# Kernel optimization log

Hardware: AMD Instinct MI355X
Metric: run time of the kernel (lower is better)

The kernel has to match this reference:

```python
import jax, jax.numpy as jnp
import numpy as np

# irreps layout: list of (multiplicity, l); same for input and output (square Linear)
IRREPS = [(256, 0), (128, 1), (64, 2)]  # dims: 256 + 384 + 320 = 960
N_NODES = 100000
N_TRIVIAL = 256  # dim of leading 0e block in irreps_out


def setup_inputs() -> dict:
    key = jax.random.key(0)
    ks = jax.random.split(key, 5)
    data_in = jax.random.normal(ks[0], (N_NODES, sum(m * (2 * l + 1) for m, l in IRREPS)), dtype=jnp.float32)
    # weight init matching linear_layer_init: uniform(-a, a), a = sqrt(6/(mul1*mul2 + mul_out)),
    # here mul1 = mul_out = mul, mul2 = 1 -> a = sqrt(6 / (2*mul)) = sqrt(3/mul)
    Ws = {}
    for i, (mul, l) in enumerate(IRREPS):
        a = float(np.sqrt(3.0 / mul))
        Ws[f"W{i}"] = jax.random.uniform(ks[i + 1], (mul, mul), minval=-a, maxval=a, dtype=jnp.float32)
    b = jnp.zeros((N_TRIVIAL,), dtype=jnp.float32)
    return {"data_in": data_in, "W0": Ws["W0"], "W1": Ws["W1"], "W2": Ws["W2"], "b": b}


def reference(data_in, W0, W1, W2, b):
    # FullyConnectedTensorProduct(irreps_in, '1x0e', irreps_out) with x2 = ones reduces to
    # per-irrep block matmul: out_block = (x_block @ W) / sqrt(mul_in)
    # (w3j(l,0,l) = I/sqrt(2l+1) cancels with component-norm sqrt((2l+1)/mul_in)).
    Ws = [W0, W1, W2]
    outs = []
    off = 0
    for (mul, l), W in zip(IRREPS, Ws):
        d = 2 * l + 1
        x = data_in[:, off : off + mul * d].reshape(-1, mul, d)  # [N, mul, 2l+1]
        y = jnp.einsum("bud,uw->bwd", x, W) * (1.0 / np.sqrt(mul))
        outs.append(y.reshape(-1, mul * d))
        off += mul * d
    out = jnp.concatenate(outs, axis=1)
    # bias added only to the leading trivial (0e) block
    out = out.at[:, :N_TRIVIAL].add(b)
    return out
```

## Files before the change

kernel.cpp:

```cpp
#include <hip/hip_runtime.h>

typedef __attribute__((ext_vector_type(8))) short short8;
typedef __attribute__((ext_vector_type(4))) float f32x4;

__device__ __forceinline__ unsigned pack2bf(float x0, float x1) {
    unsigned u0 = __float_as_uint(x0) + 0x8000u;
    unsigned u1 = __float_as_uint(x1) + 0x8000u;
    return __builtin_amdgcn_perm(u1, u0, 0x07060302u);
}

__global__ __launch_bounds__(256) void prep_w(const float* __restrict__ W,
                                              unsigned short* __restrict__ dst,
                                              int mul, float scale) {
    int idx = blockIdx.x * 256 + threadIdx.x;
    if (idx >= mul * mul) return;
    int u = idx >> (mul == 256 ? 8 : (mul == 128 ? 7 : 6));
    int w = idx - u * mul;
    int nkb = mul >> 5;
    int cb = w >> 4, kb = u >> 5;
    int lane = ((u >> 3) & 3) * 16 + (w & 15);
    int j = u & 7;
    unsigned uv = __float_as_uint(W[idx] * scale) + 0x8000u;
    dst[(((cb * nkb + kb) * 64 + lane) << 3) + j] = (unsigned short)(uv >> 16);
}

template <int MUL, int D, int OFF, bool BIAS>
__device__ __forceinline__ void do_block(const float* __restrict__ inA0,
                                         float* __restrict__ outb,
                                         const unsigned short* __restrict__ wf,
                                         int lm, int lg, int lane,
                                         const float* __restrict__ bias) {
    constexpr int NKB = MUL / 32;
    constexpr int NCB = MUL / 16;
    short8 a[D][NKB];
    const float* rowp = inA0 + OFF;
#pragma unroll
    for (int kb = 0; kb < NKB; ++kb) {
        float buf[8 * D];
        const float* p = rowp + (kb * 32 + lg * 8) * D;
#pragma unroll
        for (int v = 0; v < 2 * D; ++v) {
            f32x4 t = *reinterpret_cast<const f32x4*>(p + v * 4);
            buf[v * 4 + 0] = t[0]; buf[v * 4 + 1] = t[1];
            buf[v * 4 + 2] = t[2]; buf[v * 4 + 3] = t[3];
        }
#pragma unroll
        for (int d = 0; d < D; ++d) {
            union { short8 s8; unsigned u32[4]; } fr;
#pragma unroll
            for (int jj = 0; jj < 4; ++jj)
                fr.u32[jj] = pack2bf(buf[(2 * jj) * D + d], buf[(2 * jj + 1) * D + d]);
            a[d][kb] = fr.s8;
        }
    }
#pragma unroll 2
    for (int cb = 0; cb < NCB; ++cb) {
        short8 bfr[NKB];
#pragma unroll
        for (int kb = 0; kb < NKB; ++kb)
            bfr[kb] = *reinterpret_cast<const short8*>(wf + (((cb * NKB + kb) * 64 + lane) << 3));
        float bv = BIAS ? bias[cb * 16 + lm] : 0.0f;
        f32x4 acc[D];
#pragma unroll
        for (int d = 0; d < D; ++d) {
            f32x4 z = {0.0f, 0.0f, 0.0f, 0.0f};
#pragma unroll
            for (int kb = 0; kb < NKB; ++kb)
                z = __builtin_amdgcn_mfma_f32_16x16x32_bf16(a[d][kb], bfr[kb], z, 0, 0, 0);
            acc[d] = z;
        }
#pragma unroll
        for (int jj = 0; jj < 4; ++jj) {
            float* op = outb + (lg * 4 + jj) * 960 + OFF + (cb * 16 + lm) * D;
#pragma unroll
            for (int d = 0; d < D; ++d)
                op[d] = BIAS ? (acc[d][jj] + bv) : acc[d][jj];
        }
    }
}

__global__ __launch_bounds__(256, 4) void lin_main(const float* __restrict__ in,
                                                   const unsigned short* __restrict__ wf0,
                                                   const unsigned short* __restrict__ wf1,
                                                   const unsigned short* __restrict__ wf2,
                                                   const float* __restrict__ bias,
                                                   float* __restrict__ out) {
    int wid = blockIdx.x * 4 + (threadIdx.x >> 6);
    if (wid >= 6250) return;
    int lane = threadIdx.x & 63;
    int lm = lane & 15, lg = lane >> 4;
    int rbase = wid * 16;
    const float* inA0 = in + (size_t)(rbase + lm) * 960;
    float* outb = out + (size_t)rbase * 960;
    do_block<256, 1, 0, true >(inA0, outb, wf0, lm, lg, lane, bias);
    do_block<128, 3, 256, false>(inA0, outb, wf1, lm, lg, lane, nullptr);
    do_block<64, 5, 640, false>(inA0, outb, wf2, lm, lg, lane, nullptr);
}

extern "C" void kernel_launch(void* const* d_in, const int* in_sizes, int n_in,
                              void* d_out, int out_size, void* d_ws, size_t ws_size,
                              hipStream_t stream) {
    (void)in_sizes; (void)n_in; (void)out_size; (void)ws_size;
    const float* x  = (const float*)d_in[0];
    const float* W0 = (const float*)d_in[1];
    const float* W1 = (const float*)d_in[2];
    const float* W2 = (const float*)d_in[3];
    const float* b  = (const float*)d_in[4];
    float* out = (float*)d_out;
    unsigned short* wf = (unsigned short*)d_ws;

    prep_w<<<256, 256, 0, stream>>>(W0, wf,         256, 0.0625f);
    prep_w<<<64,  256, 0, stream>>>(W1, wf + 65536, 128, 0.08838834764831845f);
    prep_w<<<16,  256, 0, stream>>>(W2, wf + 81920, 64,  0.125f);
    lin_main<<<1563, 256, 0, stream>>>(x, wf, wf + 65536, wf + 81920, b, out);
}
```

Measured before the change: 206.5 us.

## Split irrep blocks across workgroups and keep weight column slices in registers

The single workgroup type that processed every irrep block for a 16-row tile is replaced by three groups of workgroups, one per irrep block, launched together in a grid three times larger. Each wave now holds a fixed slice of output columns' weight fragments in registers and reuses them across several row tiles, where before it reloaded every weight fragment for every tile. The cost is that input rows are read again by the waves that share a tile, which raises redundant global and cache traffic. The per-block register footprint is smaller, which could improve occupancy.

```diff
diff --git a/kernel.cpp b/kernel.cpp
--- a/kernel.cpp
+++ b/kernel.cpp
@@ -24,58 +24,22 @@
     dst[(((cb * nkb + kb) * 64 + lane) << 3) + j] = (unsigned short)(uv >> 16);
 }
 
-template <int MUL, int D, int OFF, bool BIAS>
-__device__ __forceinline__ void do_block(const float* __restrict__ inA0,
-                                         float* __restrict__ outb,
-                                         const unsigned short* __restrict__ wf,
-                                         int lm, int lg, int lane,
-                                         const float* __restrict__ bias) {
-    constexpr int NKB = MUL / 32;
-    constexpr int NCB = MUL / 16;
-    short8 a[D][NKB];
-    const float* rowp = inA0 + OFF;
+template <int D>
+__device__ __forceinline__ void pack_a(const float* __restrict__ p, short8* __restrict__ out) {
+    float buf[8 * D];
 #pragma unroll
-    for (int kb = 0; kb < NKB; ++kb) {
-        float buf[8 * D];
-        const float* p = rowp + (kb * 32 + lg * 8) * D;
+    for (int v = 0; v < 2 * D; ++v) {
+        f32x4 t = *reinterpret_cast<const f32x4*>(p + v * 4);
+        buf[v * 4 + 0] = t[0]; buf[v * 4 + 1] = t[1];
+        buf[v * 4 + 2] = t[2]; buf[v * 4 + 3] = t[3];
+    }
 #pragma unroll
-        for (int v = 0; v < 2 * D; ++v) {
-            f32x4 t = *reinterpret_cast<const f32x4*>(p + v * 4);
-            buf[v * 4 + 0] = t[0]; buf[v * 4 + 1] = t[1];
-            buf[v * 4 + 2] = t[2]; buf[v * 4 + 3] = t[3];
-        }
+    for (int d = 0; d < D; ++d) {
+        union { short8 s8; unsigned u32[4]; } fr;
 #pragma unroll
-        for (int d = 0; d < D; ++d) {
-            union { short8 s8; unsigned u32[4]; } fr;
-#pragma unroll
-            for (int jj = 0; jj < 4; ++jj)
-                fr.u32[jj] = pack2bf(buf[(2 * jj) * D + d], buf[(2 * jj + 1) * D + d]);
-            a[d][kb] = fr.s8;
-        }
-    }
-#pragma unroll 2
-    for (int cb = 0; cb < NCB; ++cb) {
-        short8 bfr[NKB];
-#pragma unroll
-        for (int kb = 0; kb < NKB; ++kb)
-            bfr[kb] = *reinterpret_cast<const short8*>(wf + (((cb * NKB + kb) * 64 + lane) << 3));
-        float bv = BIAS ? bias[cb * 16 + lm] : 0.0f;
-        f32x4 acc[D];
-#pragma unroll
-        for (int d = 0; d < D; ++d) {
-            f32x4 z = {0.0f, 0.0f, 0.0f, 0.0f};
-#pragma unroll
-            for (int kb = 0; kb < NKB; ++kb)
-                z = __builtin_amdgcn_mfma_f32_16x16x32_bf16(a[d][kb], bfr[kb], z, 0, 0, 0);
-            acc[d] = z;
-        }
-#pragma unroll
-        for (int jj = 0; jj < 4; ++jj) {
-            float* op = outb + (lg * 4 + jj) * 960 + OFF + (cb * 16 + lm) * D;
-#pragma unroll
-            for (int d = 0; d < D; ++d)
-                op[d] = BIAS ? (acc[d][jj] + bv) : acc[d][jj];
-        }
+        for (int jj = 0; jj < 4; ++jj)
+            fr.u32[jj] = pack2bf(buf[(2 * jj) * D + d], buf[(2 * jj + 1) * D + d]);
+        out[d] = fr.s8;
     }
 }
 
@@ -85,16 +49,110 @@
                                                    const unsigned short* __restrict__ wf2,
                                                    const float* __restrict__ bias,
                                                    float* __restrict__ out) {
-    int wid = blockIdx.x * 4 + (threadIdx.x >> 6);
-    if (wid >= 6250) return;
-    int lane = threadIdx.x & 63;
-    int lm = lane & 15, lg = lane >> 4;
-    int rbase = wid * 16;
-    const float* inA0 = in + (size_t)(rbase + lm) * 960;
-    float* outb = out + (size_t)rbase * 960;
-    do_block<256, 1, 0, true >(inA0, outb, wf0, lm, lg, lane, bias);
-    do_block<128, 3, 256, false>(inA0, outb, wf1, lm, lg, lane, nullptr);
-    do_block<64, 5, 640, false>(inA0, outb, wf2, lm, lg, lane, nullptr);
+    const int w = threadIdx.x >> 6;
+    const int lane = threadIdx.x & 63;
+    const int lm = lane & 15, lg = lane >> 4;
+    const int g = blockIdx.x;
+
+    if (g < 1563) {
+        short8 b[4][8];
+#pragma unroll
+        for (int c = 0; c < 4; ++c)
+#pragma unroll
+            for (int kb = 0; kb < 8; ++kb)
+                b[c][kb] = *reinterpret_cast<const short8*>(wf0 + ((((w * 4 + c) * 8 + kb) * 64 + lane) << 3));
+        float bv[4];
+#pragma unroll
+        for (int c = 0; c < 4; ++c) bv[c] = bias[(w * 4 + c) * 16 + lm];
+#pragma unroll 2
+        for (int t = 0; t < 4; ++t) {
+            int tile = g * 4 + t;
+            if (tile >= 6250) break;
+            const float* rp = in + (tile * 16 + lm) * 960;
+            short8 a[8];
+#pragma unroll
+            for (int kb = 0; kb < 8; ++kb)
+                pack_a<1>(rp + kb * 32 + lg * 8, &a[kb]);
+#pragma unroll
+            for (int c = 0; c < 4; ++c) {
+                f32x4 acc = {0.f, 0.f, 0.f, 0.f};
+#pragma unroll
+                for (int kb = 0; kb < 8; ++kb)
+                    acc = __builtin_amdgcn_mfma_f32_16x16x32_bf16(a[kb], b[c][kb], acc, 0, 0, 0);
+#pragma unroll
+                for (int jj = 0; jj < 4; ++jj)
+                    out[(tile * 16 + lg * 4 + jj) * 960 + (w * 4 + c) * 16 + lm] = acc[jj] + bv[c];
+            }
+        }
+    } else if (g < 3126) {
+        const int g1 = g - 1563, str = w >> 1, hf = w & 1;
+        short8 b[4][4];
+#pragma unroll
+        for (int c = 0; c < 4; ++c)
+#pragma unroll
+            for (int kb = 0; kb < 4; ++kb)
+                b[c][kb] = *reinterpret_cast<const short8*>(wf1 + ((((hf * 4 + c) * 4 + kb) * 64 + lane) << 3));
+#pragma unroll 2
+        for (int t = 0; t < 2; ++t) {
+            int tile = g1 * 4 + str * 2 + t;
+            if (tile >= 6250) break;
+            const float* rp = in + (tile * 16 + lm) * 960 + 256;
+            short8 a[4][3];
+#pragma unroll
+            for (int kb = 0; kb < 4; ++kb)
+                pack_a<3>(rp + (kb * 32 + lg * 8) * 3, a[kb]);
+#pragma unroll
+            for (int c = 0; c < 4; ++c) {
+                f32x4 acc[3];
+#pragma unroll
+                for (int d = 0; d < 3; ++d) acc[d] = (f32x4){0.f, 0.f, 0.f, 0.f};
+#pragma unroll
+                for (int kb = 0; kb < 4; ++kb)
+#pragma unroll
+                    for (int d = 0; d < 3; ++d)
+                        acc[d] = __builtin_amdgcn_mfma_f32_16x16x32_bf16(a[kb][d], b[c][kb], acc[d], 0, 0, 0);
+#pragma unroll
+                for (int jj = 0; jj < 4; ++jj) {
+                    float* op = out + (tile * 16 + lg * 4 + jj) * 960 + 256 + ((hf * 4 + c) * 16 + lm) * 3;
+#pragma unroll
+                    for (int d = 0; d < 3; ++d) op[d] = acc[d][jj];
+                }
+            }
+        }
+    } else {
+        const int g2 = g - 3126;
+        short8 b[4][2];
+#pragma unroll
+        for (int c = 0; c < 4; ++c)
+#pragma unroll
+            for (int kb = 0; kb < 2; ++kb)
+                b[c][kb] = *reinterpret_cast<const short8*>(wf2 + (((c * 2 + kb) * 64 + lane) << 3));
+        int tile = g2 * 4 + w;
+        if (tile < 6250) {
+            const float* rp = in + (tile * 16 + lm) * 960 + 640;
+            short8 a[2][5];
+#pragma unroll
+            for (int kb = 0; kb < 2; ++kb)
+                pack_a<5>(rp + (kb * 32 + lg * 8) * 5, a[kb]);
+#pragma unroll
+            for (int c = 0; c < 4; ++c) {
+                f32x4 acc[5];
+#pragma unroll
+                for (int d = 0; d < 5; ++d) acc[d] = (f32x4){0.f, 0.f, 0.f, 0.f};
+#pragma unroll
+                for (int kb = 0; kb < 2; ++kb)
+#pragma unroll
+                    for (int d = 0; d < 5; ++d)
+                        acc[d] = __builtin_amdgcn_mfma_f32_16x16x32_bf16(a[kb][d], b[c][kb], acc[d], 0, 0, 0);
+#pragma unroll
+                for (int jj = 0; jj < 4; ++jj) {
+                    float* op = out + (tile * 16 + lg * 4 + jj) * 960 + 640 + (c * 16 + lm) * 5;
+#pragma unroll
+                    for (int d = 0; d < 5; ++d) op[d] = acc[d][jj];
+                }
+            }
+        }
+    }
 }
 
 extern "C" void kernel_launch(void* const* d_in, const int* in_sizes, int n_in,
@@ -112,5 +170,5 @@
     prep_w<<<256, 256, 0, stream>>>(W0, wf,         256, 0.0625f);
     prep_w<<<64,  256, 0, stream>>>(W1, wf + 65536, 128, 0.08838834764831845f);
     prep_w<<<16,  256, 0, stream>>>(W2, wf + 81920, 64,  0.125f);
-    lin_main<<<1563, 256, 0, stream>>>(x, wf, wf + 65536, wf + 81920, b, out);
+    lin_main<<<4689, 256, 0, stream>>>(x, wf, wf + 65536, wf + 81920, b, out);
 }
```

Result: slower. 281.9 us (+36.5%).
